# Kernel optimization log

Measured on AMD Instinct MI355X. Metric: run time of the kernel, lower is better.

## Reference

```python
import jax, jax.numpy as jnp
import numpy as np

B, F_NODES, E = 1024, 128, 1024   # graphs, nodes/graph, edges/graph
H, HEADS = 128, 4
HD = H // HEADS


def setup_inputs() -> dict:
    key = jax.random.key(0)
    ks = jax.random.split(key, 24)
    f32 = jnp.float32
    n = jax.random.normal
    d = {
        "x": n(ks[0], (B, F_NODES), f32),
        "edge_index": jax.random.randint(ks[1], (2, E), 0, F_NODES, dtype=jnp.int32),
        # input projection Linear(1, H)
        "w_in": n(ks[2], (1, H), f32) * 0.5,
        "b_in": n(ks[3], (H,), f32) * 0.02,
        # GAT layer 0: heads=4, concat=True, per-head dim HD
        "gat0_w": n(ks[4], (H, H), f32) * (1.0 / np.sqrt(H)),
        "gat0_as": n(ks[5], (HEADS, HD), f32) * 0.1,
        "gat0_ad": n(ks[6], (HEADS, HD), f32) * 0.1,
        "gat0_b": n(ks[7], (H,), f32) * 0.02,
        "bn0_g": 1.0 + 0.1 * n(ks[8], (H,), f32),
        "bn0_b": 0.1 * n(ks[9], (H,), f32),
        "bn0_m": 0.1 * n(ks[10], (H,), f32),
        "bn0_v": 1.0 + 0.1 * jax.random.uniform(ks[11], (H,), f32),
        # GAT layer 1: heads=1, concat=False
        "gat1_w": n(ks[12], (H, H), f32) * (1.0 / np.sqrt(H)),
        "gat1_as": n(ks[13], (1, H), f32) * 0.1,
        "gat1_ad": n(ks[14], (1, H), f32) * 0.1,
        "gat1_b": n(ks[15], (H,), f32) * 0.02,
        "bn1_g": 1.0 + 0.1 * n(ks[16], (H,), f32),
        "bn1_b": 0.1 * n(ks[17], (H,), f32),
        "bn1_m": 0.1 * n(ks[18], (H,), f32),
        "bn1_v": 1.0 + 0.1 * jax.random.uniform(ks[19], (H,), f32),
        # classifier MLP H -> H//2 -> 1
        "w1": n(ks[20], (H, H // 2), f32) * (1.0 / np.sqrt(H)),
        "b1": n(ks[21], (H // 2,), f32) * 0.02,
        "w2": n(ks[22], (H // 2, 1), f32) * (1.0 / np.sqrt(H // 2)),
        "b2": n(ks[23], (1,), f32) * 0.02,
    }
    return d


def _gat(h, src, dst, N, W, a_s, a_d, b, concat):
    # PyG GATConv (shared lin for src/dst, leaky_relu slope 0.2, softmax over dst)
    heads, hd = a_s.shape
    xh = (h @ W).reshape(N, heads, hd)                      # [N, heads, hd]
    e = jax.nn.leaky_relu(
        jnp.sum(xh * a_s[None], -1)[src] + jnp.sum(xh * a_d[None], -1)[dst],
        0.2,
    )                                                        # [Etot, heads]
    m = jax.ops.segment_max(e, dst, num_segments=N)
    ex = jnp.exp(e - m[dst])
    s = jax.ops.segment_sum(ex, dst, num_segments=N)
    alpha = ex / s[dst]
    out = jax.ops.segment_sum(xh[src] * alpha[..., None], dst, num_segments=N)
    out = out.reshape(N, heads * hd) if concat else out[:, 0]
    return out + b


def _bn(h, g, b, m, v):
    return (h - m) / jnp.sqrt(v + 1e-5) * g + b


def reference(x, edge_index, w_in, b_in,
              gat0_w, gat0_as, gat0_ad, gat0_b, bn0_g, bn0_b, bn0_m, bn0_v,
              gat1_w, gat1_as, gat1_ad, gat1_b, bn1_g, bn1_b, bn1_m, bn1_v,
              w1, b1, w2, b2):
    Bsz, Fn = x.shape
    N = Bsz * Fn
    h = jax.nn.relu(x.reshape(N, 1) @ w_in + b_in)           # [N, H]
    # replicate per-graph edges with node offsets, then add self loops
    offs = jnp.arange(Bsz, dtype=edge_index.dtype) * Fn
    eib = (edge_index[:, None, :] + offs[None, :, None]).reshape(2, -1)
    loops = jnp.arange(N, dtype=edge_index.dtype)
    src = jnp.concatenate([eib[0], loops])
    dst = jnp.concatenate([eib[1], loops])
    h = _gat(h, src, dst, N, gat0_w, gat0_as, gat0_ad, gat0_b, True)
    h = jax.nn.relu(_bn(h, bn0_g, bn0_b, bn0_m, bn0_v))
    h = _gat(h, src, dst, N, gat1_w, gat1_as, gat1_ad, gat1_b, False)
    h = jax.nn.relu(_bn(h, bn1_g, bn1_b, bn1_m, bn1_v))
    # global mean pool (each graph has exactly Fn nodes)
    hp = h.reshape(Bsz, Fn, -1).mean(axis=1)                 # [B, H]
    z = jax.nn.relu(hp @ w1 + b1)
    return z @ w2 + b2                                       # [B, 1]
```

## Files before the change

### kernel.cpp

```cpp
#include <hip/hip_runtime.h>

#define FN   128
#define HDIM 128
#define NH   4
#define HSZ  32
#define EB   1024
#define ET   1152
#define RSW  132

typedef __attribute__((ext_vector_type(8))) short bf16x8;
typedef __attribute__((ext_vector_type(4))) float f32x4;
typedef unsigned int u32;
typedef unsigned short u16;

union U8 { bf16x8 v; u32 u[4]; };

__device__ __forceinline__ u32 pack_hl(float v) {
  const u32 u = __float_as_uint(v);
  const u32 hib = u & 0xFFFF0000u;
  const float lo = v - __uint_as_float(hib);
  return hib | (__float_as_uint(lo) >> 16);
}
__device__ __forceinline__ float lrelu(float v) {
  return (v > 0.f) ? v : 0.2f * v;
}

__device__ __forceinline__ void unpack_frag(const u32* __restrict__ q,
                                            bf16x8& hi, bf16x8& lo)
{
  const uint4 p0 = *(const uint4*)(q);
  const uint4 p1 = *(const uint4*)(q + 4);
  U8 H, L;
  H.u[0] = (p0.x >> 16) | (p0.y & 0xFFFF0000u);
  L.u[0] = (p0.x & 0xFFFFu) | (p0.y << 16);
  H.u[1] = (p0.z >> 16) | (p0.w & 0xFFFF0000u);
  L.u[1] = (p0.z & 0xFFFFu) | (p0.w << 16);
  H.u[2] = (p1.x >> 16) | (p1.y & 0xFFFF0000u);
  L.u[2] = (p1.x & 0xFFFFu) | (p1.y << 16);
  H.u[3] = (p1.z >> 16) | (p1.w & 0xFFFF0000u);
  L.u[3] = (p1.z & 0xFFFFu) | (p1.w << 16);
  hi = H.v; lo = L.v;
}

__global__ __launch_bounds__(256) void prep_kernel(
    const float* __restrict__ g0w, const float* __restrict__ g1w,
    const int* __restrict__ ei,
    u16* __restrict__ wf, u16* __restrict__ csrS, int* __restrict__ csrI)
{
  if (blockIdx.x == 128) {
    __shared__ int deg[FN], rp[FN + 1], fill[FN];
    __shared__ u16 eb[ET];
    const int t = threadIdx.x;
    if (t < FN) { deg[t] = 0; fill[t] = 0; }
    __syncthreads();
    for (int e = t; e < EB; e += 256) atomicAdd(&deg[ei[EB + e]], 1);
    __syncthreads();
    if (t < 64) {
      const int v0 = deg[2 * t] + 1, v1 = deg[2 * t + 1] + 1;
      const int p = v0 + v1;
      int sc = p;
      #pragma unroll
      for (int off = 1; off < 64; off <<= 1) {
        const int o = __shfl_up(sc, off, 64);
        if (t >= off) sc += o;
      }
      rp[2 * t] = sc - p;
      rp[2 * t + 1] = sc - v1;
      if (t == 63) rp[128] = sc;
    }
    __syncthreads();
    if (t < FN) {
      const int dn = deg[t];
      int rk = 0;
      for (int m = 0; m < FN; ++m) {
        const int dm = deg[m];
        rk += (dm > dn) || (dm == dn && m < t);
      }
      csrI[129 + rk] = t;
      csrI[t] = rp[t];
      if (t == 0) csrI[FN] = rp[FN];
    }
    __syncthreads();
    for (int e = t; e < EB; e += 256) {
      const int d = ei[EB + e], s = ei[e];
      const int p = rp[d] + atomicAdd(&fill[d], 1);
      eb[p] = (u16)s;
    }
    if (t < FN) eb[rp[t] + deg[t]] = (u16)t;
    __syncthreads();
    if (t < FN) {
      const int e0 = rp[t], e1 = rp[t] + deg[t] + 1;
      for (int i = e0 + 1; i < e1; ++i) {
        const u16 v = eb[i];
        const int kv = ((int)v - t) & 7;
        int j = i - 1;
        while (j >= e0 && (((int)eb[j] - t) & 7) > kv) { eb[j + 1] = eb[j]; --j; }
        eb[j + 1] = v;
      }
    }
    __syncthreads();
    for (int e = t; e < ET; e += 256) csrS[e] = eb[e];
    return;
  }

  const int idx = blockIdx.x * 256 + threadIdx.x;
  const int layer = idx >> 14;
  const int r = idx & 16383;
  const int c  = r >> 11;
  const int kc = (r >> 9) & 3;
  const int l  = (r >> 3) & 63;
  const int j  = r & 7;
  const int k = kc * 32 + (l >> 4) * 8 + j;
  const int n = c * 16 + (l & 15);
  const float* W = layer ? g1w : g0w;
  const float v = W[k * HDIM + n];
  const u32 u = __float_as_uint(v);
  const u32 hib = u & 0xFFFF0000u;
  const float lo = v - __uint_as_float(hib);
  wf[layer * 32768 + r]         = (u16)(u >> 16);
  wf[layer * 32768 + 16384 + r] = (u16)(__float_as_uint(lo) >> 16);
}

__device__ __forceinline__ void mfma_gemm_acc(const u32* __restrict__ F,
                                              const u16* __restrict__ wf,
                                              int lw, int lane, f32x4 acc[4][2])
{
  const int cg = lw & 3, rh = lw >> 2;
  const int m = lane & 15, quad = lane >> 4;

  #pragma unroll
  for (int s = 0; s < 4; ++s)
    #pragma unroll
    for (int ct = 0; ct < 2; ++ct) acc[s][ct] = (f32x4){0.f, 0.f, 0.f, 0.f};

  const u16* bbase = wf + (cg * 8) * 512 + lane * 8;

  #pragma unroll
  for (int kc = 0; kc < 4; ++kc) {
    bf16x8 bhi[2], blo[2];
    #pragma unroll
    for (int ct = 0; ct < 2; ++ct) {
      const u16* bp = bbase + ct * 2048 + kc * 512;
      bhi[ct] = *(const bf16x8*)bp;
      blo[ct] = *(const bf16x8*)(bp + 16384);
    }
    #pragma unroll
    for (int s = 0; s < 4; ++s) {
      const u32* ap = F + (rh * 64 + s * 16 + m) * RSW + quad * 8 + kc * 32;
      bf16x8 ahi, alo;
      unpack_frag(ap, ahi, alo);
      #pragma unroll
      for (int ct = 0; ct < 2; ++ct) {
        acc[s][ct] = __builtin_amdgcn_mfma_f32_16x16x32_bf16(ahi, bhi[ct], acc[s][ct], 0, 0, 0);
        acc[s][ct] = __builtin_amdgcn_mfma_f32_16x16x32_bf16(alo, bhi[ct], acc[s][ct], 0, 0, 0);
        acc[s][ct] = __builtin_amdgcn_mfma_f32_16x16x32_bf16(ahi, blo[ct], acc[s][ct], 0, 0, 0);
      }
    }
  }
}

__device__ __forceinline__ void store_acc(float* __restrict__ sg, int lw,
                                          int lane, const f32x4 acc[4][2])
{
  const int cg = lw & 3, rh = lw >> 2;
  const int m = lane & 15, quad = lane >> 4;
  #pragma unroll
  for (int s = 0; s < 4; ++s) {
    const int row0 = rh * 64 + s * 16 + quad * 4;
    #pragma unroll
    for (int ct = 0; ct < 2; ++ct)
      #pragma unroll
      for (int r = 0; r < 4; ++r)
        sg[(row0 + r) * RSW + cg * 32 + ct * 16 + m] = acc[s][ct][r];
  }
}

__global__ __launch_bounds__(512, 4) void gnn_fused_kernel(
    const float* __restrict__ x,
    const float* __restrict__ w_in, const float* __restrict__ b_in,
    const float* __restrict__ g0as, const float* __restrict__ g0ad,
    const float* __restrict__ g0b,
    const float* __restrict__ bn0g, const float* __restrict__ bn0b,
    const float* __restrict__ bn0m, const float* __restrict__ bn0v,
    const float* __restrict__ g1as, const float* __restrict__ g1ad,
    const float* __restrict__ g1b,
    const float* __restrict__ bn1g, const float* __restrict__ bn1b,
    const float* __restrict__ bn1m, const float* __restrict__ bn1v,
    const float* __restrict__ w1, const float* __restrict__ b1,
    const float* __restrict__ w2, const float* __restrict__ b2,
    const u16* __restrict__ wf, const u16* __restrict__ csrS,
    const int* __restrict__ csrI,
    float* __restrict__ out)
{
  __shared__ u32   F[FN * RSW];
  __shared__ int   s_rp[FN + 1];
  __shared__ int   s_perm[FN];
  __shared__ u16   s_src[ET];
  __shared__ float s_scr[1280];
  __shared__ float s_bn[512];

  const int t = threadIdx.x;
  const int gid = blockIdx.x;
  const int lane = t & 63;
  const int lw = t >> 6;
  float* s_es = s_scr;
  float* s_ed = s_scr + 512;
  float* s_rs = s_scr + 1024;
  f32x4 acc[4][2];

  for (int w = t; w < ET / 2; w += 512)
    ((u32*)s_src)[w] = ((const u32*)csrS)[w];
  if (t < FN + 1) s_rp[t] = csrI[t];
  if (t < FN)     s_perm[t] = csrI[129 + t];
  if (t >= 256 && t < 512) {
    const int layer = (t >> 7) & 1;
    const int col = t & 127;
    const float bb = layer ? g1b[col]  : g0b[col];
    const float bm = layer ? bn1m[col] : bn0m[col];
    const float bv = layer ? bn1v[col] : bn0v[col];
    const float bg = layer ? bn1g[col] : bn0g[col];
    const float bt = layer ? bn1b[col] : bn0b[col];
    const float q = bg * rsqrtf(bv + 1e-5f);
    s_bn[layer * 256 + col] = q;
    s_bn[layer * 256 + 128 + col] = (bb - bm) * q + bt;
  }
  {
    const int j = t & 127, q = t >> 7;
    const float wv = w_in[j], bv = b_in[j];
    const size_t xb = (size_t)gid * FN;
    for (int n = q * 32; n < q * 32 + 32; ++n) {
      const float v = fmaxf(fmaf(x[xb + n], wv, bv), 0.f);
      F[n * RSW + j] = pack_hl(v);
    }
  }
  __syncthreads();

  mfma_gemm_acc(F, wf, lw, lane, acc);
  __syncthreads();
  store_acc((float*)F, lw, lane, acc);
  __syncthreads();

  {
    const int hh = t >> 7, n = t & 127;
    const float* row = (const float*)F + n * RSW + hh * HSZ;
    float accs = 0.f, accd = 0.f;
    #pragma unroll
    for (int s = 0; s < 8; ++s) {
      const int d = ((n + s) & 7) * 4;
      const float4 v  = *(const float4*)(row + d);
      const float4 as = *(const float4*)(g0as + hh * HSZ + d);
      const float4 ad = *(const float4*)(g0ad + hh * HSZ + d);
      accs += v.x*as.x + v.y*as.y + v.z*as.z + v.w*as.w;
      accd += v.x*ad.x + v.y*ad.y + v.z*ad.z + v.w*ad.w;
    }
    s_es[hh * 128 + n] = accs;
    s_ed[hh * 128 + n] = accd;
  }
  __syncthreads();

  {
    const int slot = t & 127, hh = t >> 7;
    const int n = s_perm[slot];
    const int cb = hh * HSZ;
    const float* Ff = (const float*)F;
    const int e0 = s_rp[n], e1 = s_rp[n + 1];
    const float edv = s_ed[hh * 128 + n];
    const float* esb = s_es + hh * 128;
    float sum = 0.f;
    float4 a[8];
    #pragma unroll
    for (int i = 0; i < 8; ++i) a[i] = make_float4(0.f, 0.f, 0.f, 0.f);
    for (int e = e0; e < e1; ++e) {
      const int s = s_src[e];
      const float al = __expf(lrelu(esb[s] + edv));
      sum += al;
      const float* rp_ = Ff + s * RSW + cb;
      #pragma unroll
      for (int i = 0; i < 8; ++i) {
        const float4 vv = *(const float4*)(rp_ + i * 4);
        a[i].x = fmaf(al, vv.x, a[i].x); a[i].y = fmaf(al, vv.y, a[i].y);
        a[i].z = fmaf(al, vv.z, a[i].z); a[i].w = fmaf(al, vv.w, a[i].w);
      }
    }
    const float rsv = 1.f / sum;
    __syncthreads();
    #pragma unroll
    for (int i = 0; i < 8; ++i) {
      const int col = cb + i * 4;
      const float4 q = *(const float4*)&s_bn[col];
      const float4 r = *(const float4*)&s_bn[128 + col];
      uint4 p;
      p.x = pack_hl(fmaxf(fmaf(a[i].x * rsv, q.x, r.x), 0.f));
      p.y = pack_hl(fmaxf(fmaf(a[i].y * rsv, q.y, r.y), 0.f));
      p.z = pack_hl(fmaxf(fmaf(a[i].z * rsv, q.z, r.z), 0.f));
      p.w = pack_hl(fmaxf(fmaf(a[i].w * rsv, q.w, r.w), 0.f));
      *(uint4*)(F + n * RSW + col) = p;
    }
  }
  __syncthreads();

  mfma_gemm_acc(F, wf + 32768, lw, lane, acc);
  __syncthreads();
  store_acc((float*)F, lw, lane, acc);
  __syncthreads();

  {
    const int n = t >> 2, c = t & 3;
    const float* row = (const float*)F + n * RSW + c * 32;
    float accs = 0.f, accd = 0.f;
    #pragma unroll
    for (int i = 0; i < 8; ++i) {
      const int d = i * 4;
      const float4 v  = *(const float4*)(row + d);
      const float4 as = *(const float4*)(g1as + c * 32 + d);
      const float4 ad = *(const float4*)(g1ad + c * 32 + d);
      accs += v.x*as.x + v.y*as.y + v.z*as.z + v.w*as.w;
      accd += v.x*ad.x + v.y*ad.y + v.z*ad.z + v.w*ad.w;
    }
    s_es[t] = accs;
    s_ed[t] = accd;
  }
  __syncthreads();
  if (t < 128) {
    const float* pe = s_es + t * 4;
    const float* pd = s_ed + t * 4;
    s_rs[t]       = pe[0] + pe[1] + pe[2] + pe[3];
    s_rs[128 + t] = pd[0] + pd[1] + pd[2] + pd[3];
  }
  __syncthreads();

  {
    const int slot = t & 127, cg = t >> 7;
    const int cb = cg * HSZ;
    const int n = s_perm[slot];
    const float* Ff = (const float*)F;
    const int e0 = s_rp[n], e1 = s_rp[n + 1];
    const float edv = s_rs[128 + n];
    float sum = 0.f;
    float4 a[8];
    #pragma unroll
    for (int i = 0; i < 8; ++i) a[i] = make_float4(0.f, 0.f, 0.f, 0.f);
    for (int e = e0; e < e1; ++e) {
      const int s = s_src[e];
      const float al = __expf(lrelu(s_rs[s] + edv));
      sum += al;
      const float* rp_ = Ff + s * RSW + cb;
      #pragma unroll
      for (int i = 0; i < 8; ++i) {
        const float4 vv = *(const float4*)(rp_ + i * 4);
        a[i].x = fmaf(al, vv.x, a[i].x); a[i].y = fmaf(al, vv.y, a[i].y);
        a[i].z = fmaf(al, vv.z, a[i].z); a[i].w = fmaf(al, vv.w, a[i].w);
      }
    }
    const float rsv = 1.f / sum;
    __syncthreads();
    #pragma unroll
    for (int i = 0; i < 8; ++i) {
      const int col = cb + i * 4;
      const float4 q = *(const float4*)&s_bn[256 + col];
      const float4 r = *(const float4*)&s_bn[384 + col];
      uint4 p;
      p.x = __float_as_uint(fmaxf(fmaf(a[i].x * rsv, q.x, r.x), 0.f));
      p.y = __float_as_uint(fmaxf(fmaf(a[i].y * rsv, q.y, r.y), 0.f));
      p.z = __float_as_uint(fmaxf(fmaf(a[i].z * rsv, q.z, r.z), 0.f));
      p.w = __float_as_uint(fmaxf(fmaf(a[i].w * rsv, q.w, r.w), 0.f));
      *(uint4*)(F + n * RSW + col) = p;
    }
  }
  __syncthreads();

  {
    const int j = t & 127, q = t >> 7;
    float p = 0.f;
    for (int n = q * 32; n < q * 32 + 32; ++n)
      p += __uint_as_float(F[n * RSW + j]);
    s_es[q * 128 + j] = p;
  }
  __syncthreads();
  if (t < 128) {
    s_ed[t] = (s_es[t] + s_es[t + 128] + s_es[t + 256] + s_es[t + 384])
              * (1.f / 128.f);
  }
  __syncthreads();
  {
    const int j = t & 63, part = t >> 6;
    float a = 0.f;
    #pragma unroll
    for (int k = part * 16; k < part * 16 + 16; ++k)
      a = fmaf(s_ed[k], w1[k * 64 + j], a);
    s_es[part * 64 + j] = a;
  }
  __syncthreads();
  if (t < 64) {
    float a = b1[t];
    #pragma unroll
    for (int p = 0; p < 8; ++p) a += s_es[p * 64 + t];
    a = fmaxf(a, 0.f);
    float v = a * w2[t];
    #pragma unroll
    for (int off = 32; off > 0; off >>= 1) v += __shfl_down(v, off, 64);
    if (t == 0) out[gid] = v + b2[0];
  }
}

extern "C" void kernel_launch(void* const* d_in, const int* in_sizes, int n_in,
                              void* d_out, int out_size, void* d_ws, size_t ws_size,
                              hipStream_t stream)
{
  const float* x    = (const float*)d_in[0];
  const int*   ei   = (const int*)d_in[1];
  const float* w_in = (const float*)d_in[2];
  const float* b_in = (const float*)d_in[3];
  const float* g0w  = (const float*)d_in[4];
  const float* g0as = (const float*)d_in[5];
  const float* g0ad = (const float*)d_in[6];
  const float* g0b  = (const float*)d_in[7];
  const float* bn0g = (const float*)d_in[8];
  const float* bn0b = (const float*)d_in[9];
  const float* bn0m = (const float*)d_in[10];
  const float* bn0v = (const float*)d_in[11];
  const float* g1w  = (const float*)d_in[12];
  const float* g1as = (const float*)d_in[13];
  const float* g1ad = (const float*)d_in[14];
  const float* g1b  = (const float*)d_in[15];
  const float* bn1g = (const float*)d_in[16];
  const float* bn1b = (const float*)d_in[17];
  const float* bn1m = (const float*)d_in[18];
  const float* bn1v = (const float*)d_in[19];
  const float* w1   = (const float*)d_in[20];
  const float* b1   = (const float*)d_in[21];
  const float* w2   = (const float*)d_in[22];
  const float* b2   = (const float*)d_in[23];

  u16* wf   = (u16*)d_ws;
  u16* csrS = (u16*)((char*)d_ws + 131072);
  int* csrI = (int*)((char*)d_ws + 131072 + 2304);

  prep_kernel<<<129, 256, 0, stream>>>(g0w, g1w, ei, wf, csrS, csrI);
  gnn_fused_kernel<<<1024, 512, 0, stream>>>(x, w_in, b_in,
      g0as, g0ad, g0b, bn0g, bn0b, bn0m, bn0v,
      g1as, g1ad, g1b, bn1g, bn1b, bn1m, bn1v,
      w1, b1, w2, b2, wf, csrS, csrI, (float*)d_out);
}
```

Measured before the change: 193.1 us.

## Store GEMM A-operand as separate bf16 hi/lo planes in LDS

Node features for the MFMA GEMMs are now written to shared memory as two planes of packed bf16 pairs, one holding the high halves and one the low-residual halves, with row stride 68. The GEMM then loads its hi and lo fragments directly, with no per-fragment unpack shuffles. The prep kernel drops the per-destination edge insertion sort, which ordered edges to spread bank access, and writes CSR sources straight to global memory. The attention-logit read swizzle also changes. Removing the sort may bring back LDS bank conflicts during neighbor aggregation.

Result: faster. 173.3 us (-10.3%).

```diff
diff --git a/kernel.cpp b/kernel.cpp
--- a/kernel.cpp
+++ b/kernel.cpp
@@ -7,39 +7,27 @@
 #define EB   1024
 #define ET   1152
 #define RSW  132
+#define RSP  68
+#define PLO  (FN * RSP)
 
 typedef __attribute__((ext_vector_type(8))) short bf16x8;
 typedef __attribute__((ext_vector_type(4))) float f32x4;
 typedef unsigned int u32;
 typedef unsigned short u16;
 
-union U8 { bf16x8 v; u32 u[4]; };
-
-__device__ __forceinline__ u32 pack_hl(float v) {
-  const u32 u = __float_as_uint(v);
-  const u32 hib = u & 0xFFFF0000u;
-  const float lo = v - __uint_as_float(hib);
-  return hib | (__float_as_uint(lo) >> 16);
-}
 __device__ __forceinline__ float lrelu(float v) {
   return (v > 0.f) ? v : 0.2f * v;
 }
 
-__device__ __forceinline__ void unpack_frag(const u32* __restrict__ q,
-                                            bf16x8& hi, bf16x8& lo)
-{
-  const uint4 p0 = *(const uint4*)(q);
-  const uint4 p1 = *(const uint4*)(q + 4);
-  U8 H, L;
-  H.u[0] = (p0.x >> 16) | (p0.y & 0xFFFF0000u);
-  L.u[0] = (p0.x & 0xFFFFu) | (p0.y << 16);
-  H.u[1] = (p0.z >> 16) | (p0.w & 0xFFFF0000u);
-  L.u[1] = (p0.z & 0xFFFFu) | (p0.w << 16);
-  H.u[2] = (p1.x >> 16) | (p1.y & 0xFFFF0000u);
-  L.u[2] = (p1.x & 0xFFFFu) | (p1.y << 16);
-  H.u[3] = (p1.z >> 16) | (p1.w & 0xFFFF0000u);
-  L.u[3] = (p1.z & 0xFFFFu) | (p1.w << 16);
-  hi = H.v; lo = L.v;
+__device__ __forceinline__ void split_pair(float v0, float v1,
+                                           u32& hw, u32& lw_)
+{
+  const u32 u0 = __float_as_uint(v0), u1 = __float_as_uint(v1);
+  const u32 h0 = u0 & 0xFFFF0000u,  h1 = u1 & 0xFFFF0000u;
+  const float l0 = v0 - __uint_as_float(h0);
+  const float l1 = v1 - __uint_as_float(h1);
+  hw  = (h0 >> 16) | h1;
+  lw_ = (__float_as_uint(l0) >> 16) | (__float_as_uint(l1) & 0xFFFF0000u);
 }
 
 __global__ __launch_bounds__(256) void prep_kernel(
@@ -49,7 +37,6 @@
 {
   if (blockIdx.x == 128) {
     __shared__ int deg[FN], rp[FN + 1], fill[FN];
-    __shared__ u16 eb[ET];
     const int t = threadIdx.x;
     if (t < FN) { deg[t] = 0; fill[t] = 0; }
     __syncthreads();
@@ -84,22 +71,9 @@
     for (int e = t; e < EB; e += 256) {
       const int d = ei[EB + e], s = ei[e];
       const int p = rp[d] + atomicAdd(&fill[d], 1);
-      eb[p] = (u16)s;
-    }
-    if (t < FN) eb[rp[t] + deg[t]] = (u16)t;
-    __syncthreads();
-    if (t < FN) {
-      const int e0 = rp[t], e1 = rp[t] + deg[t] + 1;
-      for (int i = e0 + 1; i < e1; ++i) {
-        const u16 v = eb[i];
-        const int kv = ((int)v - t) & 7;
-        int j = i - 1;
-        while (j >= e0 && (((int)eb[j] - t) & 7) > kv) { eb[j + 1] = eb[j]; --j; }
-        eb[j + 1] = v;
-      }
-    }
-    __syncthreads();
-    for (int e = t; e < ET; e += 256) csrS[e] = eb[e];
+      csrS[p] = (u16)s;
+    }
+    if (t < FN) csrS[rp[t] + deg[t]] = (u16)t;
     return;
   }
 
@@ -146,9 +120,9 @@
     }
     #pragma unroll
     for (int s = 0; s < 4; ++s) {
-      const u32* ap = F + (rh * 64 + s * 16 + m) * RSW + quad * 8 + kc * 32;
-      bf16x8 ahi, alo;
-      unpack_frag(ap, ahi, alo);
+      const u32* ap = F + (rh * 64 + s * 16 + m) * RSP + quad * 4 + kc * 16;
+      const bf16x8 ahi = *(const bf16x8*)ap;
+      const bf16x8 alo = *(const bf16x8*)(ap + PLO);
       #pragma unroll
       for (int ct = 0; ct < 2; ++ct) {
         acc[s][ct] = __builtin_amdgcn_mfma_f32_16x16x32_bf16(ahi, bhi[ct], acc[s][ct], 0, 0, 0);
@@ -192,7 +166,7 @@
     const int* __restrict__ csrI,
     float* __restrict__ out)
 {
-  __shared__ u32   F[FN * RSW];
+  __shared__ __align__(16) u32 F[2 * FN * RSP];
   __shared__ int   s_rp[FN + 1];
   __shared__ int   s_perm[FN];
   __shared__ u16   s_src[ET];
@@ -225,12 +199,19 @@
     s_bn[layer * 256 + 128 + col] = (bb - bm) * q + bt;
   }
   {
-    const int j = t & 127, q = t >> 7;
-    const float wv = w_in[j], bv = b_in[j];
+    const int j2 = t & 63, q = t >> 6;
+    const int c0 = 2 * j2, c1 = c0 + 1;
+    const float w0 = w_in[c0], b0 = b_in[c0];
+    const float w1v = w_in[c1], b1v = b_in[c1];
     const size_t xb = (size_t)gid * FN;
-    for (int n = q * 32; n < q * 32 + 32; ++n) {
-      const float v = fmaxf(fmaf(x[xb + n], wv, bv), 0.f);
-      F[n * RSW + j] = pack_hl(v);
+    for (int n = q * 16; n < q * 16 + 16; ++n) {
+      const float xv = x[xb + n];
+      const float v0 = fmaxf(fmaf(xv, w0, b0), 0.f);
+      const float v1 = fmaxf(fmaf(xv, w1v, b1v), 0.f);
+      u32 hw, lw_;
+      split_pair(v0, v1, hw, lw_);
+      F[n * RSP + j2]       = hw;
+      F[PLO + n * RSP + j2] = lw_;
     }
   }
   __syncthreads();
@@ -246,7 +227,7 @@
     float accs = 0.f, accd = 0.f;
     #pragma unroll
     for (int s = 0; s < 8; ++s) {
-      const int d = ((n + s) & 7) * 4;
+      const int d = ((s + (n >> 3)) & 7) * 4;
       const float4 v  = *(const float4*)(row + d);
       const float4 as = *(const float4*)(g0as + hh * HSZ + d);
       const float4 ad = *(const float4*)(g0ad + hh * HSZ + d);
@@ -289,12 +270,16 @@
       const int col = cb + i * 4;
       const float4 q = *(const float4*)&s_bn[col];
       const float4 r = *(const float4*)&s_bn[128 + col];
-      uint4 p;
-      p.x = pack_hl(fmaxf(fmaf(a[i].x * rsv, q.x, r.x), 0.f));
-      p.y = pack_hl(fmaxf(fmaf(a[i].y * rsv, q.y, r.y), 0.f));
-      p.z = pack_hl(fmaxf(fmaf(a[i].z * rsv, q.z, r.z), 0.f));
-      p.w = pack_hl(fmaxf(fmaf(a[i].w * rsv, q.w, r.w), 0.f));
-      *(uint4*)(F + n * RSW + col) = p;
+      const float vx = fmaxf(fmaf(a[i].x * rsv, q.x, r.x), 0.f);
+      const float vy = fmaxf(fmaf(a[i].y * rsv, q.y, r.y), 0.f);
+      const float vz = fmaxf(fmaf(a[i].z * rsv, q.z, r.z), 0.f);
+      const float vw = fmaxf(fmaf(a[i].w * rsv, q.w, r.w), 0.f);
+      u32 h0, l0, h1, l1;
+      split_pair(vx, vy, h0, l0);
+      split_pair(vz, vw, h1, l1);
+      const int wi = n * RSP + (cb >> 1) + i * 2;
+      *(uint2*)(F + wi)       = make_uint2(h0, h1);
+      *(uint2*)(F + PLO + wi) = make_uint2(l0, l1);
     }
   }
   __syncthreads();
```
